# Kernel optimization log

Measured on AMD Instinct MI355X. Metric: run time of the kernel, lower is better.

Reference implementation:

```python
import jax, jax.numpy as jnp
import numpy as np

N, S, M = 16, 256, 768
TK, HA = 10, 1          # tK stages, hA heads (from RTM.__init__)
DH = M // HA
EPS = 1e-5
WSCALE = 0.02           # scale on randn weights to keep 10 stacked stages numerically sane


def _pos_bias():
    # bias[i][j][z] = sin(j / 10000**(2z/M)), bias[i][j][z+1] = cos(...); independent of i
    pos = np.arange(S, dtype=np.float64)[:, None]
    z = np.arange(0, M, 2, dtype=np.float64)
    ang = pos / (10000.0 ** (2.0 * z / M))          # (S, M/2)
    pe = np.zeros((S, M), dtype=np.float32)
    pe[:, 0::2] = np.sin(ang)
    pe[:, 1::2] = np.cos(ang)
    return jnp.asarray(pe)

PE = _pos_bias()


def _ln(v, g, b):
    mu = jnp.mean(v, axis=-1, keepdims=True)
    var = jnp.var(v, axis=-1, keepdims=True)
    return (v - mu) / jnp.sqrt(var + EPS) * g + b


def setup_inputs() -> dict:
    key = jax.random.key(0)
    ks = jax.random.split(key, 8)
    rn = lambda k, shp: jax.random.normal(k, shp, dtype=jnp.float32)
    return {
        "x": rn(ks[0], (N, S, M)),
        "weight": rn(ks[1], (M, M)) * WSCALE,
        "Wq": rn(ks[2], (TK, HA, DH, M)) * WSCALE,
        "Wk": rn(ks[3], (TK, HA, DH, M)) * WSCALE,
        "Wv": rn(ks[4], (TK, HA, DH, M)) * WSCALE,
        "Wo": rn(ks[5], (TK, M, M)) * WSCALE,
        "ln1_g": jnp.ones((M,), jnp.float32), "ln1_b": jnp.zeros((M,), jnp.float32),
        "ln2_g": jnp.ones((M,), jnp.float32), "ln2_b": jnp.zeros((M,), jnp.float32),
        "fc1_w": rn(ks[6], (4 * M, M)) * WSCALE, "fc1_b": jnp.zeros((4 * M,), jnp.float32),
        "fc2_w": rn(ks[7], (M, 4 * M)) * WSCALE, "fc2_b": jnp.zeros((M,), jnp.float32),
    }


def reference(x, weight, Wq, Wk, Wv, Wo, ln1_g, ln1_b, ln2_g, ln2_b,
              fc1_w, fc1_b, fc2_w, fc2_b):
    # savespace[i,j] = weight @ x[i,j,:]  (x[j,:,i] after the double transpose), + sin/cos bias
    s0 = jnp.einsum('mn,ijn->ijm', weight, x) + PE[None, :, :]   # (N, S, M)
    inv_sqrt_dh = jnp.float32(1.0 / np.sqrt(DH))

    def mlp(s):
        h = jax.nn.gelu(s @ fc1_w.T + fc1_b, approximate=False)
        return h @ fc2_w.T + fc2_b

    # Sequential over tokens j: token j attends (strictly causal) to the per-stage V
    # of all previous tokens, accumulated in cumV. Within a token, the tK stages run
    # sequentially, each mutating the token's state s (as the torch code mutates savespace).
    def token_step(cumV, s):                # cumV: (TK, N, HA, DH); s: (N, M)
        newV = []
        for a in range(TK):
            sn = _ln(s, ln1_g, ln1_b)
            q = jnp.einsum('hdm,nm->nhd', Wq[a], sn)
            k = jnp.einsum('hdm,nm->nhd', Wk[a], sn)
            v = jnp.einsum('hdm,nm->nhd', Wv[a], sn)
            logit = jnp.sum(q * inv_sqrt_dh * k, axis=-1)                # (N, HA) scalar score
            rsa = jax.nn.softmax(logit[..., None], axis=-1)[..., 0]      # softmax of scalar == 1
            imv = cumV[a]                                                # (N, HA, DH): sum_{subj<j}
            s = jnp.einsum('mk,nk->nm', Wo[a], imv.reshape(N, HA * DH)) + s
            s = _ln(s, ln2_g, ln2_b) + s
            s = mlp(s)
            newV.append(rsa[..., None] * v)
        return cumV + jnp.stack(newV, axis=0), s

    cumV0 = jnp.zeros((TK, N, HA, DH), x.dtype)
    _, ys = jax.lax.scan(token_step, cumV0, jnp.swapaxes(s0, 0, 1))      # ys: (S, N, M)
    return jnp.swapaxes(ys, 0, 1)                                        # (N, S, M)
```

## Files before the change

### kernel.cpp

```cpp
#include <hip/hip_runtime.h>
#include <hip/hip_bf16.h>
#include <math.h>


using bf16   = __bf16;
using bf16x8 = __attribute__((ext_vector_type(8))) __bf16;
using f32x4  = __attribute__((ext_vector_type(4))) float;

#define DEV __device__ __forceinline__

DEV void gload16(const bf16* g, bf16* l) {
  __builtin_amdgcn_global_load_lds(
      (const __attribute__((address_space(1))) unsigned int*)g,
      (__attribute__((address_space(3))) unsigned int*)l, 16, 0, 0);
}

DEV float gelu_f(float x) {
  const float y  = x * 0.70710678118654752f;
  const float ay = fabsf(y);
  const float t  = __builtin_amdgcn_rcpf(__builtin_fmaf(0.3275911f, ay, 1.0f));
  float p = __builtin_fmaf(1.061405429f, t, -1.453152027f);
  p = __builtin_fmaf(p, t, 1.421413741f);
  p = __builtin_fmaf(p, t, -0.284496736f);
  p = __builtin_fmaf(p, t, 0.254829592f);
  p = p * t;
  const float e = __expf(-ay * ay);
  float er = __builtin_fmaf(-p, e, 1.0f);
  er = __builtin_copysignf(er, y);
  return 0.5f * x * (1.0f + er);
}

enum { EPI_PART = 0, EPI_GELU = 1, EPI_B16 = 2 };

template <int BN, int EPI>
__global__ __launch_bounds__(256) void gemm_k(
    const bf16* __restrict__ A, const bf16* __restrict__ B,
    float* __restrict__ outF, bf16* __restrict__ outB,
    const float* __restrict__ aux, int K, int N,
    int kZ, int klen, size_t aZ, size_t bZ, size_t oZ)
{
  constexpr int ABUF = 128 * 32;
  constexpr int BBUF = BN * 32;
  __shared__ bf16 As[2 * ABUF];
  __shared__ bf16 Bs[2 * BBUF];
  const int z = blockIdx.z;
  A += (size_t)z * aZ;
  B += (size_t)z * bZ;
  const int kbeg = z * kZ;
  const int tid  = threadIdx.x;
  const int lane = tid & 63, wave = tid >> 6;
  const int m0 = blockIdx.x * 128, n0 = blockIdx.y * BN;

  const int r  = tid >> 2;
  const int kq = ((tid & 3) - (tid >> 3)) & 3;
  const bf16* aG0 = A + (size_t)(m0 + r) * K + kq * 8 + kbeg;
  const bf16* aG1 = aG0 + (size_t)64 * K;
  const bf16* bG0 = B + (size_t)(n0 + r) * K + kq * 8 + kbeg;
  const bf16* bG1 = bG0 + (size_t)64 * K;

  const int wr = (wave & 1) * 64, wc = (wave >> 1) * (BN / 2);
  const int lr = lane & 15, kb = lane >> 4;
  const int swz  = ((kb + (lr >> 1)) & 3) * 8;
  const int aOff = (wr + lr) * 32 + swz;
  const int bOff = (wc + lr) * 32 + swz;

  constexpr int MT = 4, NT = BN / 32;
  f32x4 acc[MT][NT] = {};
  const int iters = klen >> 5;

  auto stage = [&](int p, int k0) {
    bf16* aD = &As[p * ABUF + tid * 8];
    gload16(aG0 + k0, aD);
    gload16(aG1 + k0, aD + 2048);
    bf16* bD = &Bs[p * BBUF + tid * 8];
    gload16(bG0 + k0, bD);
    if (BN == 128) gload16(bG1 + k0, bD + 2048);
  };

  stage(0, 0);
  for (int it = 0; it < iters; ++it) {
    __syncthreads();
    if (it + 1 < iters) stage((it + 1) & 1, (it + 1) * 32);
    const int pa = (it & 1) * ABUF, pb = (it & 1) * BBUF;
    bf16x8 af[MT], bfv[NT];
#pragma unroll
    for (int t = 0; t < MT; ++t) af[t] = *(const bf16x8*)&As[pa + aOff + t * 512];
#pragma unroll
    for (int t = 0; t < NT; ++t) bfv[t] = *(const bf16x8*)&Bs[pb + bOff + t * 512];
#pragma unroll
    for (int mt = 0; mt < MT; ++mt)
#pragma unroll
      for (int nt = 0; nt < NT; ++nt)
        acc[mt][nt] = __builtin_amdgcn_mfma_f32_16x16x32_bf16(af[mt], bfv[nt], acc[mt][nt], 0, 0, 0);
  }

  const int row0 = m0 + wr + (lane >> 4) * 4;
  const int col0 = n0 + wc + lr;
  float* oF = (EPI == EPI_PART) ? outF + (size_t)z * oZ : nullptr;
  bf16*  oB = (EPI == EPI_B16)  ? outB + (size_t)z * oZ : outB;
#pragma unroll
  for (int mt = 0; mt < MT; ++mt) {
#pragma unroll
    for (int nt = 0; nt < NT; ++nt) {
      const int col = col0 + nt * 16;
      float bias = 0.f;
      if (EPI == EPI_GELU) bias = aux[col];
#pragma unroll
      for (int rg = 0; rg < 4; ++rg) {
        const int row = row0 + mt * 16 + rg;
        float v = acc[mt][nt][rg];
        if (EPI == EPI_PART) {
          oF[(size_t)row * N + col] = v;
        } else if (EPI == EPI_GELU) {
          oB[(size_t)row * N + col] = (bf16)gelu_f(v + bias);
        } else {
          oB[(size_t)row * N + col] = (bf16)v;
        }
      }
    }
  }
}

template <int NP, int MODE>
__global__ __launch_bounds__(256) void reduce_ln(
    const float* __restrict__ P, size_t pZ,
    const float* __restrict__ add, const float* __restrict__ g,
    const float* __restrict__ b, float* __restrict__ Tout,
    bf16* __restrict__ SNout)
{
  const int row = blockIdx.x, t = threadIdx.x;
  float v[3];
#pragma unroll
  for (int c = 0; c < 3; ++c) {
    const int col = t + c * 256;
    float s = P[(size_t)row * 768 + col];
#pragma unroll
    for (int p = 1; p < NP; ++p) s += P[(size_t)p * pZ + (size_t)row * 768 + col];
    if (MODE == 0) s += add[(row & 255) * 768 + col];
    if (MODE == 1) s += add[(size_t)row * 768 + col];
    if (MODE == 2 || MODE == 3) s += add[col];
    v[c] = s;
  }
  if (MODE != 1) {
#pragma unroll
    for (int c = 0; c < 3; ++c) Tout[(size_t)row * 768 + t + c * 256] = v[c];
  }
  if (MODE == 3) return;

  __shared__ float red[8];
  float s = v[0] + v[1] + v[2];
#pragma unroll
  for (int o = 32; o >= 1; o >>= 1) s += __shfl_down(s, o);
  if ((t & 63) == 0) red[t >> 6] = s;
  __syncthreads();
  const float mu = (red[0] + red[1] + red[2] + red[3]) * (1.f / 768.f);
  const float d0 = v[0] - mu, d1 = v[1] - mu, d2 = v[2] - mu;
  float q = d0 * d0 + d1 * d1 + d2 * d2;
#pragma unroll
  for (int o = 32; o >= 1; o >>= 1) q += __shfl_down(q, o);
  if ((t & 63) == 0) red[4 + (t >> 6)] = q;
  __syncthreads();
  const float var = (red[4] + red[5] + red[6] + red[7]) * (1.f / 768.f);
  const float rs = rsqrtf(var + 1e-5f);
  float y0 = d0 * rs * g[t] + b[t];
  float y1 = d1 * rs * g[t + 256] + b[t + 256];
  float y2 = d2 * rs * g[t + 512] + b[t + 512];
  if (MODE == 1) { y0 += v[0]; y1 += v[1]; y2 += v[2]; }
  bf16* o = SNout + (size_t)row * 768;
  o[t] = (bf16)y0; o[t + 256] = (bf16)y1; o[t + 512] = (bf16)y2;
}

__global__ __launch_bounds__(256) void scan_partial_b(
    const bf16* __restrict__ SN, float* __restrict__ Ps)
{
  const int n = blockIdx.x, ch = blockIdx.y, d = blockIdx.z * 256 + threadIdx.x;
  const bf16* base = SN + ((size_t)(n * 256 + ch * 16)) * 768 + d;
  float s = 0.f;
#pragma unroll
  for (int j = 0; j < 16; ++j) s += (float)base[(size_t)j * 768];
  Ps[(size_t)(n * 16 + ch) * 768 + d] = s;
}

__global__ __launch_bounds__(256) void scan_final_b(
    const bf16* __restrict__ SN, const float* __restrict__ Ps,
    bf16* __restrict__ PSb)
{
  const int n = blockIdx.x, ch = blockIdx.y, d = blockIdx.z * 256 + threadIdx.x;
  float run = 0.f;
  for (int c = 0; c < ch; ++c) run += Ps[(size_t)(n * 16 + c) * 768 + d];
  const bf16* vb = SN + ((size_t)(n * 256 + ch * 16)) * 768 + d;
  bf16* ob = PSb + ((size_t)(n * 256 + ch * 16)) * 768 + d;
#pragma unroll
  for (int j = 0; j < 16; ++j) {
    ob[(size_t)j * 768] = (bf16)run;
    run += (float)vb[(size_t)j * 768];
  }
}

__global__ __launch_bounds__(256) void transpose_wv(
    const float* __restrict__ Wv, bf16* __restrict__ WvT)
{
  __shared__ float tile[64][65];
  const int a = blockIdx.z, k0 = blockIdx.x * 64, n0 = blockIdx.y * 64;
  const int c = threadIdx.x & 63, r4 = threadIdx.x >> 6;
  const float* src = Wv + (size_t)a * 589824;
  bf16* dst = WvT + (size_t)a * 589824;
#pragma unroll
  for (int i = 0; i < 16; ++i)
    tile[r4 + i * 4][c] = src[(size_t)(k0 + r4 + i * 4) * 768 + n0 + c];
  __syncthreads();
#pragma unroll
  for (int i = 0; i < 16; ++i) {
    const int n = r4 + i * 4;
    dst[(size_t)(n0 + n) * 768 + k0 + c] = (bf16)tile[c][n];
  }
}

__global__ __launch_bounds__(256) void f32_to_bf16_k(
    const float* __restrict__ in, bf16* __restrict__ out, int n4)
{
  const int i = blockIdx.x * 256 + threadIdx.x;
  if (i >= n4) return;
  const float4 v = ((const float4*)in)[i];
  bf16 h[4] = {(bf16)v.x, (bf16)v.y, (bf16)v.z, (bf16)v.w};
  *(uint2*)(out + 4 * (size_t)i) = *(uint2*)h;
}

__global__ __launch_bounds__(256) void pe_kernel(float* __restrict__ PE)
{
  const int id = blockIdx.x * 256 + threadIdx.x;
  const int j = id / 384, p = id % 384;
  const double ang = (double)j * pow(10000.0, -4.0 * (double)p / 768.0);
  PE[(size_t)j * 768 + 2 * p]     = (float)sin(ang);
  PE[(size_t)j * 768 + 2 * p + 1] = (float)cos(ang);
}

extern "C" void kernel_launch(void* const* d_in, const int* in_sizes, int n_in,
                              void* d_out, int out_size, void* d_ws, size_t ws_size,
                              hipStream_t stream)
{
  const float* x      = (const float*)d_in[0];
  const float* weight = (const float*)d_in[1];
  const float* Wv     = (const float*)d_in[4];
  const float* Wo     = (const float*)d_in[5];
  const float* ln1g   = (const float*)d_in[6];
  const float* ln1b   = (const float*)d_in[7];
  const float* ln2g   = (const float*)d_in[8];
  const float* ln2b   = (const float*)d_in[9];
  const float* fc1w   = (const float*)d_in[10];
  const float* fc1b   = (const float*)d_in[11];
  const float* fc2w   = (const float*)d_in[12];
  const float* fc2b   = (const float*)d_in[13];
  float* out = (float*)d_out;

  char* p = (char*)d_ws;
  auto alloc = [&](size_t bytes) { char* r = p; p += (bytes + 255) & ~(size_t)255; return r; };
  bf16*  Wb_w  = (bf16*)alloc(589824ull * 2);
  bf16*  Wb_o  = (bf16*)alloc(5898240ull * 2);
  bf16*  WvT   = (bf16*)alloc(5898240ull * 2);
  bf16*  Wvo   = (bf16*)alloc(5898240ull * 2);
  bf16*  Wb_f1 = (bf16*)alloc(2359296ull * 2);
  bf16*  Wb_f2 = (bf16*)alloc(2359296ull * 2);
  bf16*  Xb    = (bf16*)alloc(3145728ull * 2);
  float* PEf   = (float*)alloc(196608ull * 4);
  float* T     = (float*)alloc(3145728ull * 4);
  bf16*  SN    = (bf16*)alloc(3145728ull * 2);
  bf16*  PSb   = (bf16*)alloc(3145728ull * 2);
  bf16*  H     = (bf16*)alloc(12582912ull * 2);
  float* Ps    = (float*)alloc(196608ull * 4);
  float* Part  = (float*)alloc(2ull * 3145728ull * 4);

  auto cvt = [&](const float* src, bf16* dst, int n) {
    int n4 = n / 4;
    f32_to_bf16_k<<<(n4 + 255) / 256, 256, 0, stream>>>(src, dst, n4);
  };
  cvt(x, Xb, 3145728);
  cvt(weight, Wb_w, 589824);
  cvt(Wo, Wb_o, 5898240);
  cvt(fc1w, Wb_f1, 2359296);
  cvt(fc2w, Wb_f2, 2359296);
  transpose_wv<<<dim3(12, 12, 10), 256, 0, stream>>>(Wv, WvT);
  pe_kernel<<<384, 256, 0, stream>>>(PEf);

  gemm_k<128, EPI_B16><<<dim3(6, 6, 10), 256, 0, stream>>>(
      Wb_o, WvT, nullptr, Wvo, nullptr, 768, 768, 0, 768, 589824, 589824, 589824);

  gemm_k<64, EPI_PART><<<dim3(32, 12, 2), 256, 0, stream>>>(
      Xb, Wb_w, Part, nullptr, nullptr, 768, 768, 384, 384, 0, 0, 3145728);
  reduce_ln<2, 0><<<4096, 256, 0, stream>>>(Part, 3145728, PEf, ln1g, ln1b, T, SN);

  for (int a = 0; a < 10; ++a) {
    scan_partial_b<<<dim3(16, 16, 3), 256, 0, stream>>>(SN, Ps);
    scan_final_b<<<dim3(16, 16, 3), 256, 0, stream>>>(SN, Ps, PSb);
    gemm_k<64, EPI_PART><<<dim3(32, 12, 2), 256, 0, stream>>>(
        PSb, Wvo + (size_t)a * 589824, Part, nullptr, nullptr, 768, 768, 384, 384, 0, 0, 3145728);
    reduce_ln<2, 1><<<4096, 256, 0, stream>>>(Part, 3145728, T, ln2g, ln2b, nullptr, SN);
    gemm_k<128, EPI_GELU><<<dim3(32, 24, 1), 256, 0, stream>>>(
        SN, Wb_f1, nullptr, H, fc1b, 768, 3072, 0, 768, 0, 0, 0);
    gemm_k<64, EPI_PART><<<dim3(32, 12, 2), 256, 0, stream>>>(
        H, Wb_f2, Part, nullptr, nullptr, 3072, 768, 1536, 1536, 0, 0, 3145728);
    if (a < 9)
      reduce_ln<2, 2><<<4096, 256, 0, stream>>>(Part, 3145728, fc2b, ln1g, ln1b, T, SN);
    else
      reduce_ln<2, 3><<<4096, 256, 0, stream>>>(Part, 3145728, fc2b, nullptr, nullptr, out, nullptr);
  }
  (void)in_sizes; (void)n_in; (void)out_size; (void)ws_size;
}
```

Measured before the change: 1.253 ms.

## Load GEMM fragments directly from global memory and use a single-pass scan

Replaces the LDS-staged, double-buffered GEMM with a variant where each wave loads its MFMA fragments straight from global memory into registers, ping-ponging two register sets, with a transposed tile shape and a launch-bounds occupancy hint. This drops shared memory and barriers but relies on L1/L2 to serve the redundant per-wave loads. The two-kernel chunked prefix scan is also replaced by one kernel where each thread walks all 256 tokens serially, removing a launch and the partial-sum buffer at the cost of far fewer threads (48 blocks) doing a long serial loop.

```diff
diff --git a/kernel.cpp b/kernel.cpp
--- a/kernel.cpp
+++ b/kernel.cpp
@@ -8,12 +8,6 @@
 using f32x4  = __attribute__((ext_vector_type(4))) float;
 
 #define DEV __device__ __forceinline__
-
-DEV void gload16(const bf16* g, bf16* l) {
-  __builtin_amdgcn_global_load_lds(
-      (const __attribute__((address_space(1))) unsigned int*)g,
-      (__attribute__((address_space(3))) unsigned int*)l, 16, 0, 0);
-}
 
 DEV float gelu_f(float x) {
   const float y  = x * 0.70710678118654752f;
@@ -32,66 +26,57 @@
 
 enum { EPI_PART = 0, EPI_GELU = 1, EPI_B16 = 2 };
 
-template <int BN, int EPI>
-__global__ __launch_bounds__(256) void gemm_k(
+template <int BM, int EPI>
+__global__ __launch_bounds__(256, 3) void gemm_d(
     const bf16* __restrict__ A, const bf16* __restrict__ B,
     float* __restrict__ outF, bf16* __restrict__ outB,
     const float* __restrict__ aux, int K, int N,
     int kZ, int klen, size_t aZ, size_t bZ, size_t oZ)
 {
-  constexpr int ABUF = 128 * 32;
-  constexpr int BBUF = BN * 32;
-  __shared__ bf16 As[2 * ABUF];
-  __shared__ bf16 Bs[2 * BBUF];
+  constexpr int MT = BM / 32;
+  constexpr int NT = 4;
   const int z = blockIdx.z;
   A += (size_t)z * aZ;
   B += (size_t)z * bZ;
   const int kbeg = z * kZ;
   const int tid  = threadIdx.x;
   const int lane = tid & 63, wave = tid >> 6;
-  const int m0 = blockIdx.x * 128, n0 = blockIdx.y * BN;
-
-  const int r  = tid >> 2;
-  const int kq = ((tid & 3) - (tid >> 3)) & 3;
-  const bf16* aG0 = A + (size_t)(m0 + r) * K + kq * 8 + kbeg;
-  const bf16* aG1 = aG0 + (size_t)64 * K;
-  const bf16* bG0 = B + (size_t)(n0 + r) * K + kq * 8 + kbeg;
-  const bf16* bG1 = bG0 + (size_t)64 * K;
-
-  const int wr = (wave & 1) * 64, wc = (wave >> 1) * (BN / 2);
+  const int m0 = blockIdx.x * BM, n0 = blockIdx.y * 128;
+  const int wr = (wave & 1) * (BM / 2), wc = (wave >> 1) * 64;
   const int lr = lane & 15, kb = lane >> 4;
-  const int swz  = ((kb + (lr >> 1)) & 3) * 8;
-  const int aOff = (wr + lr) * 32 + swz;
-  const int bOff = (wc + lr) * 32 + swz;
-
-  constexpr int MT = 4, NT = BN / 32;
+
+  const bf16* aP[MT];
+  const bf16* bP[NT];
+#pragma unroll
+  for (int t = 0; t < MT; ++t)
+    aP[t] = A + (size_t)(m0 + wr + t * 16 + lr) * K + kb * 8 + kbeg;
+#pragma unroll
+  for (int t = 0; t < NT; ++t)
+    bP[t] = B + (size_t)(n0 + wc + t * 16 + lr) * K + kb * 8 + kbeg;
+
   f32x4 acc[MT][NT] = {};
-  const int iters = klen >> 5;
-
-  auto stage = [&](int p, int k0) {
-    bf16* aD = &As[p * ABUF + tid * 8];
-    gload16(aG0 + k0, aD);
-    gload16(aG1 + k0, aD + 2048);
-    bf16* bD = &Bs[p * BBUF + tid * 8];
-    gload16(bG0 + k0, bD);
-    if (BN == 128) gload16(bG1 + k0, bD + 2048);
+  bf16x8 aA[MT], bA[NT], aB[MT], bB[NT];
+
+  auto ldfrag = [&](bf16x8* af, bf16x8* bf, int k) {
+#pragma unroll
+    for (int t = 0; t < MT; ++t) af[t] = *(const bf16x8*)(aP[t] + k);
+#pragma unroll
+    for (int t = 0; t < NT; ++t) bf[t] = *(const bf16x8*)(bP[t] + k);
   };
-
-  stage(0, 0);
-  for (int it = 0; it < iters; ++it) {
-    __syncthreads();
-    if (it + 1 < iters) stage((it + 1) & 1, (it + 1) * 32);
-    const int pa = (it & 1) * ABUF, pb = (it & 1) * BBUF;
-    bf16x8 af[MT], bfv[NT];
-#pragma unroll
-    for (int t = 0; t < MT; ++t) af[t] = *(const bf16x8*)&As[pa + aOff + t * 512];
-#pragma unroll
-    for (int t = 0; t < NT; ++t) bfv[t] = *(const bf16x8*)&Bs[pb + bOff + t * 512];
+  auto domfma = [&](bf16x8* af, bf16x8* bf) {
 #pragma unroll
     for (int mt = 0; mt < MT; ++mt)
 #pragma unroll
       for (int nt = 0; nt < NT; ++nt)
-        acc[mt][nt] = __builtin_amdgcn_mfma_f32_16x16x32_bf16(af[mt], bfv[nt], acc[mt][nt], 0, 0, 0);
+        acc[mt][nt] = __builtin_amdgcn_mfma_f32_16x16x32_bf16(af[mt], bf[nt], acc[mt][nt], 0, 0, 0);
+  };
+
+  ldfrag(aA, bA, 0);
+  for (int k0 = 0; k0 < klen; k0 += 64) {
+    ldfrag(aB, bB, k0 + 32);
+    domfma(aA, bA);
+    if (k0 + 64 < klen) ldfrag(aA, bA, k0 + 64);
+    domfma(aB, bB);
   }
 
   const int row0 = m0 + wr + (lane >> 4) * 4;
@@ -170,30 +155,18 @@
   o[t] = (bf16)y0; o[t + 256] = (bf16)y1; o[t + 512] = (bf16)y2;
 }
 
-__global__ __launch_bounds__(256) void scan_partial_b(
-    const bf16* __restrict__ SN, float* __restrict__ Ps)
-{
-  const int n = blockIdx.x, ch = blockIdx.y, d = blockIdx.z * 256 + threadIdx.x;
-  const bf16* base = SN + ((size_t)(n * 256 + ch * 16)) * 768 + d;
-  float s = 0.f;
-#pragma unroll
-  for (int j = 0; j < 16; ++j) s += (float)base[(size_t)j * 768];
-  Ps[(size_t)(n * 16 + ch) * 768 + d] = s;
-}
-
-__global__ __launch_bounds__(256) void scan_final_b(
-    const bf16* __restrict__ SN, const float* __restrict__ Ps,
-    bf16* __restrict__ PSb)
-{
-  const int n = blockIdx.x, ch = blockIdx.y, d = blockIdx.z * 256 + threadIdx.x;
+__global__ __launch_bounds__(256) void scan_k(
+    const bf16* __restrict__ SN, bf16* __restrict__ PSb)
+{
+  const int n = blockIdx.x, d = blockIdx.y * 256 + threadIdx.x;
+  const bf16* s = SN + (size_t)n * 256 * 768 + d;
+  bf16* o = PSb + (size_t)n * 256 * 768 + d;
   float run = 0.f;
-  for (int c = 0; c < ch; ++c) run += Ps[(size_t)(n * 16 + c) * 768 + d];
-  const bf16* vb = SN + ((size_t)(n * 256 + ch * 16)) * 768 + d;
-  bf16* ob = PSb + ((size_t)(n * 256 + ch * 16)) * 768 + d;
-#pragma unroll
-  for (int j = 0; j < 16; ++j) {
-    ob[(size_t)j * 768] = (bf16)run;
-    run += (float)vb[(size_t)j * 768];
+#pragma unroll 8
+  for (int j = 0; j < 256; ++j) {
+    const float v = (float)s[(size_t)j * 768];
+    o[(size_t)j * 768] = (bf16)run;
+    run += v;
   }
 }
 
@@ -267,7 +240,6 @@
   bf16*  SN    = (bf16*)alloc(3145728ull * 2);
   bf16*  PSb   = (bf16*)alloc(3145728ull * 2);
   bf16*  H     = (bf16*)alloc(12582912ull * 2);
-  float* Ps    = (float*)alloc(196608ull * 4);
   float* Part  = (float*)alloc(2ull * 3145728ull * 4);
 
   auto cvt = [&](const float* src, bf16* dst, int n) {
@@ -282,22 +254,21 @@
   transpose_wv<<<dim3(12, 12, 10), 256, 0, stream>>>(Wv, WvT);
   pe_kernel<<<384, 256, 0, stream>>>(PEf);
 
-  gemm_k<128, EPI_B16><<<dim3(6, 6, 10), 256, 0, stream>>>(
+  gemm_d<64, EPI_B16><<<dim3(12, 6, 10), 256, 0, stream>>>(
       Wb_o, WvT, nullptr, Wvo, nullptr, 768, 768, 0, 768, 589824, 589824, 589824);
 
-  gemm_k<64, EPI_PART><<<dim3(32, 12, 2), 256, 0, stream>>>(
+  gemm_d<64, EPI_PART><<<dim3(64, 6, 2), 256, 0, stream>>>(
       Xb, Wb_w, Part, nullptr, nullptr, 768, 768, 384, 384, 0, 0, 3145728);
   reduce_ln<2, 0><<<4096, 256, 0, stream>>>(Part, 3145728, PEf, ln1g, ln1b, T, SN);
 
   for (int a = 0; a < 10; ++a) {
-    scan_partial_b<<<dim3(16, 16, 3), 256, 0, stream>>>(SN, Ps);
-    scan_final_b<<<dim3(16, 16, 3), 256, 0, stream>>>(SN, Ps, PSb);
-    gemm_k<64, EPI_PART><<<dim3(32, 12, 2), 256, 0, stream>>>(
+    scan_k<<<dim3(16, 3), 256, 0, stream>>>(SN, PSb);
+    gemm_d<64, EPI_PART><<<dim3(64, 6, 2), 256, 0, stream>>>(
         PSb, Wvo + (size_t)a * 589824, Part, nullptr, nullptr, 768, 768, 384, 384, 0, 0, 3145728);
     reduce_ln<2, 1><<<4096, 256, 0, stream>>>(Part, 3145728, T, ln2g, ln2b, nullptr, SN);
-    gemm_k<128, EPI_GELU><<<dim3(32, 24, 1), 256, 0, stream>>>(
+    gemm_d<128, EPI_GELU><<<dim3(32, 24, 1), 256, 0, stream>>>(
         SN, Wb_f1, nullptr, H, fc1b, 768, 3072, 0, 768, 0, 0, 0);
-    gemm_k<64, EPI_PART><<<dim3(32, 12, 2), 256, 0, stream>>>(
+    gemm_d<64, EPI_PART><<<dim3(64, 6, 2), 256, 0, stream>>>(
         H, Wb_f2, Part, nullptr, nullptr, 3072, 768, 1536, 1536, 0, 0, 3145728);
     if (a < 9)
       reduce_ln<2, 2><<<4096, 256, 0, stream>>>(Part, 3145728, fc2b, ln1g, ln1b, T, SN);
```

After: 2.628 ms. 2.1x slower.
